# Optimization experiments

Measured on AMD Instinct MI355X. Metric: run time of the kernel, lower is better.

## Reference

```python
import jax, jax.numpy as jnp
import numpy as np


def setup_inputs() -> dict:
    key = jax.random.key(0)
    k1, k2, k3 = jax.random.split(key, 3)
    B, Nin, Din, Nout, Dout = 32, 512, 64, 32, 64
    w_const = float(np.sqrt(Nout / (Din * Nin)))  # weight_init_const from module
    return {
        "input_pose": jax.random.normal(k1, (B, Nin, Din), dtype=jnp.float32),
        "current_act": jax.random.uniform(k2, (B, Nin), dtype=jnp.float32),
        "W": w_const * jax.random.normal(k3, (Nin, Din, Nout, Dout), dtype=jnp.float32),
        "num_iter": 3,
    }


def reference(input_pose, current_act, W, num_iter):
    # input_pose: [B, Nin, Din], current_act: [B, Nin], W: [Nin, Din, Nout, Dout]
    Nin, Din, Nout, Dout = W.shape
    scale = 1.0 / np.sqrt(Dout)

    # Vote projection is iteration-invariant: compute once.  [B, Nin, Nout, Dout]
    votes = jnp.einsum('bna,namd->bnmd', input_pose, W)

    # Initial pass: q0 = softmax(zeros) = uniform 1/Nout over classes.
    # einsum('nm,bna,namd->bmd', q0, pose, W) == votes.sum(n) / Nout
    next_capsule_value = votes.sum(axis=1) / Nout  # [B, Nout, Dout]

    query_key = None
    for _ in range(max(1, num_iter)):
        # 'bna,namd,bmd->bnm' == contraction of cached votes with current class poses
        logits = jnp.einsum('bnmd,bmd->bnm', votes, next_capsule_value) * scale
        query_key = jax.nn.softmax(logits, axis=2)  # [B, Nin, Nout]
        # 'bnm,bna,namd,bn->bmd' == activation-weighted vote aggregation
        next_capsule_value = jnp.einsum('bnm,bnmd,bn->bmd', query_key, votes, current_act)

    # act_type == 'EM' and next_act is None -> pose L2 norm
    next_act = jnp.linalg.norm(next_capsule_value, axis=-1)  # [B, Nout]

    # per-route x per-class interaction embeddings  [B, Nin, Nout, Dout]
    weights = query_key * current_act[..., None]
    route_class_emb = weights[..., None] * votes

    return next_capsule_value, next_act, query_key, route_class_emb
```

## Files before the change

kernel.cpp:

```cpp
#include <hip/hip_runtime.h>

#define B_    32
#define NIN   512
#define DIN   64
#define NOUT  32
#define DOUT  64
#define NUM_ITER 3

__global__ __launch_bounds__(128) void k_votes(const float* __restrict__ pose,
                                               const float* __restrict__ W,
                                               float* __restrict__ votes) {
    const int n = blockIdx.x >> 5;
    const int m = blockIdx.x & 31;
    const int tid = threadIdx.x;
    const int d4 = tid & 15;
    const int bq = tid >> 4;

    __shared__ float poseL[B_ * 68];
#pragma unroll
    for (int k = 0; k < 4; ++k) {
        int j = tid + k * 128;
        int b = j >> 4, a4 = j & 15;
        float4 v = *((const float4*)(pose + (size_t)(b * NIN + n) * DIN) + a4);
        *(float4*)&poseL[b * 68 + a4 * 4] = v;
    }
    __syncthreads();

    const float4* wp = (const float4*)W + (size_t)n * 32768 + m * 16 + d4;
    const float* p0 = &poseL[(bq * 4 + 0) * 68];
    const float* p1 = p0 + 68;
    const float* p2 = p1 + 68;
    const float* p3 = p2 + 68;

    float4 a0 = {0.f,0.f,0.f,0.f}, a1 = {0.f,0.f,0.f,0.f};
    float4 a2 = {0.f,0.f,0.f,0.f}, a3 = {0.f,0.f,0.f,0.f};
#pragma unroll 16
    for (int a = 0; a < 64; ++a) {
        float4 wv = wp[(size_t)a * 512];
        float q0 = p0[a], q1 = p1[a], q2 = p2[a], q3 = p3[a];
        a0.x = fmaf(q0, wv.x, a0.x); a0.y = fmaf(q0, wv.y, a0.y);
        a0.z = fmaf(q0, wv.z, a0.z); a0.w = fmaf(q0, wv.w, a0.w);
        a1.x = fmaf(q1, wv.x, a1.x); a1.y = fmaf(q1, wv.y, a1.y);
        a1.z = fmaf(q1, wv.z, a1.z); a1.w = fmaf(q1, wv.w, a1.w);
        a2.x = fmaf(q2, wv.x, a2.x); a2.y = fmaf(q2, wv.y, a2.y);
        a2.z = fmaf(q2, wv.z, a2.z); a2.w = fmaf(q2, wv.w, a2.w);
        a3.x = fmaf(q3, wv.x, a3.x); a3.y = fmaf(q3, wv.y, a3.y);
        a3.z = fmaf(q3, wv.z, a3.z); a3.w = fmaf(q3, wv.w, a3.w);
    }
    float4* vo = (float4*)votes + ((size_t)(bq * 4) * NIN + n) * 512 + m * 16 + d4;
    const size_t bs = (size_t)NIN * 512;
    vo[0]      = a0;
    vo[bs]     = a1;
    vo[2 * bs] = a2;
    vo[3 * bs] = a3;
}

__global__ __launch_bounds__(256) void k_ncv0(const float* __restrict__ votes,
                                              float* __restrict__ ncv) {
    int gid = blockIdx.x * 256 + threadIdx.x;
    int nc = gid >> 16;
    int e  = gid & 65535;
    int b  = e >> 11;
    int r  = e & 2047;
    const float* vp = votes + (size_t)b * (NIN * 2048) + (size_t)nc * 64 * 2048 + r;
    float s = 0.f;
#pragma unroll 8
    for (int nn = 0; nn < 64; ++nn) s += vp[nn * 2048];
    atomicAdd(&ncv[e], s * (1.0f / NOUT));
}

__global__ __launch_bounds__(256) void k_iter(float* __restrict__ votes,
                                              const float* __restrict__ act,
                                              const float* __restrict__ ncv_in,
                                              float* __restrict__ ncv_out,
                                              float* __restrict__ qk_out,
                                              int last) {
    const int b = blockIdx.x >> 5;
    const int chunk = blockIdx.x & 31;
    const int tid = threadIdx.x;
    const int wave = tid >> 6, lane = tid & 63;
    const int m = lane & 31, half = lane >> 5;
    const int sl = m * 64 + half * 32;

    const float4* np = (const float4*)(ncv_in + (size_t)b * 2048 + sl);
    float4 ncvs[8];
#pragma unroll
    for (int i = 0; i < 8; ++i) ncvs[i] = np[i];

    float4 acc[8];
#pragma unroll
    for (int i = 0; i < 8; ++i) acc[i] = make_float4(0.f, 0.f, 0.f, 0.f);

    const int n0 = chunk * 16 + wave * 4;

    for (int nn = 0; nn < 4; ++nn) {
        const int n = n0 + nn;
        float4* vp = (float4*)(votes + (size_t)(b * NIN + n) * 2048 + sl);
        float4 v[8];
#pragma unroll
        for (int i = 0; i < 8; ++i) v[i] = vp[i];

        float part = 0.f;
#pragma unroll
        for (int i = 0; i < 8; ++i) {
            part = fmaf(v[i].x, ncvs[i].x, part);
            part = fmaf(v[i].y, ncvs[i].y, part);
            part = fmaf(v[i].z, ncvs[i].z, part);
            part = fmaf(v[i].w, ncvs[i].w, part);
        }
        part += __shfl_xor(part, 32);
        float lg = part * 0.125f;

        float mx = lg;
#pragma unroll
        for (int off = 16; off >= 1; off >>= 1) mx = fmaxf(mx, __shfl_xor(mx, off));
        float e = __expf(lg - mx);
        float s = e;
#pragma unroll
        for (int off = 16; off >= 1; off >>= 1) s += __shfl_xor(s, off);
        float qk = e / s;
        if (half == 0) qk_out[(size_t)(b * NIN + n) * NOUT + m] = qk;

        const float qa = qk * act[b * NIN + n];
#pragma unroll
        for (int i = 0; i < 8; ++i) {
            acc[i].x = fmaf(qa, v[i].x, acc[i].x);
            acc[i].y = fmaf(qa, v[i].y, acc[i].y);
            acc[i].z = fmaf(qa, v[i].z, acc[i].z);
            acc[i].w = fmaf(qa, v[i].w, acc[i].w);
        }
        if (last) {
#pragma unroll
            for (int i = 0; i < 8; ++i) {
                float4 ev;
                ev.x = qa * v[i].x; ev.y = qa * v[i].y;
                ev.z = qa * v[i].z; ev.w = qa * v[i].w;
                vp[i] = ev;
            }
        }
    }

    __shared__ float accW[4][64 * 33];
    const int lid = m * 2 + half;
    float* aw = &accW[wave][lid * 33];
#pragma unroll
    for (int i = 0; i < 8; ++i) {
        aw[4 * i + 0] = acc[i].x; aw[4 * i + 1] = acc[i].y;
        aw[4 * i + 2] = acc[i].z; aw[4 * i + 3] = acc[i].w;
    }
    __syncthreads();
    for (int e = tid; e < 2048; e += 256) {
        int mm = e >> 6, dd = e & 63;
        int idx = (mm * 2 + (dd >> 5)) * 33 + (dd & 31);
        float s = accW[0][idx] + accW[1][idx] + accW[2][idx] + accW[3][idx];
        atomicAdd(&ncv_out[(size_t)b * 2048 + e], s);
    }
}

__global__ __launch_bounds__(256) void k_final_ncv(const float* __restrict__ ncv,
                                                   float* __restrict__ ncv_out,
                                                   float* __restrict__ act_out) {
    int gid = blockIdx.x * 256 + threadIdx.x;
    ncv_out[gid] = ncv[gid];
    if (gid < B_ * NOUT) {
        const float* p = ncv + gid * DOUT;
        float s = 0.f;
#pragma unroll 8
        for (int d = 0; d < DOUT; ++d) s = fmaf(p[d], p[d], s);
        act_out[gid] = sqrtf(s);
    }
}

extern "C" void kernel_launch(void* const* d_in, const int* in_sizes, int n_in,
                              void* d_out, int out_size, void* d_ws, size_t ws_size,
                              hipStream_t stream) {
    const float* pose = (const float*)d_in[0];
    const float* act  = (const float*)d_in[1];
    const float* W    = (const float*)d_in[2];

    float* out = (float*)d_out;
    float* ncv_out = out;
    float* act_out = out + 65536;
    float* qk_out  = out + 66560;
    float* emb_out = out + 590848;

    char* ws = (char*)d_ws;
    float* ncvA = (float*)ws;
    float* ncvB = (float*)(ws + 262144);

    float* votes = emb_out;

    k_votes<<<NIN * NOUT, 128, 0, stream>>>(pose, W, votes);

    hipMemsetAsync(ncvA, 0, B_ * NOUT * DOUT * sizeof(float), stream);
    k_ncv0<<<2048, 256, 0, stream>>>(votes, ncvA);

    float* cur = ncvA;
    float* nxt = ncvB;
    for (int it = 0; it < NUM_ITER; ++it) {
        hipMemsetAsync(nxt, 0, B_ * NOUT * DOUT * sizeof(float), stream);
        k_iter<<<B_ * 32, 256, 0, stream>>>(votes, act, cur, nxt, qk_out,
                                            it == NUM_ITER - 1 ? 1 : 0);
        float* t = cur; cur = nxt; nxt = t;
    }

    k_final_ncv<<<256, 256, 0, stream>>>(cur, ncv_out, act_out);
}
```

Before: 617.6 us.

## Retile vote projection kernel by capsule and batch group with larger register tiles

The votes kernel now gives each block one input capsule and a group of 8 batch elements covering all 32 output classes. Each thread computes an 8-batch by 8-dim register tile and loads the pose vector as float4. The block index is permuted so blocks sharing the same n (and thus the same W slice) run on different XCDs or close in time. W is now read four times per capsule instead of once per (n,m) block over all 32 batches, trading W reuse for fewer blocks and larger per-thread tiles, with higher register pressure.

Result: faster. 585.4 us (-5.2%).

```diff
diff --git a/kernel.cpp b/kernel.cpp
--- a/kernel.cpp
+++ b/kernel.cpp
@@ -7,52 +7,71 @@
 #define DOUT  64
 #define NUM_ITER 3
 
-__global__ __launch_bounds__(128) void k_votes(const float* __restrict__ pose,
+__global__ __launch_bounds__(256) void k_votes(const float* __restrict__ pose,
                                                const float* __restrict__ W,
                                                float* __restrict__ votes) {
-    const int n = blockIdx.x >> 5;
-    const int m = blockIdx.x & 31;
+    const int logical = (blockIdx.x & 7) * 256 + (blockIdx.x >> 3);
+    const int n  = logical >> 2;
+    const int b0 = (logical & 3) * 8;
     const int tid = threadIdx.x;
-    const int d4 = tid & 15;
-    const int bq = tid >> 4;
-
-    __shared__ float poseL[B_ * 68];
-#pragma unroll
-    for (int k = 0; k < 4; ++k) {
-        int j = tid + k * 128;
-        int b = j >> 4, a4 = j & 15;
-        float4 v = *((const float4*)(pose + (size_t)(b * NIN + n) * DIN) + a4);
-        *(float4*)&poseL[b * 68 + a4 * 4] = v;
+    const int m  = tid >> 3;
+    const int d8 = tid & 7;
+
+    __shared__ float poseL[8 * 64];
+    if (tid < 128) {
+        int bb = tid >> 4, a4 = tid & 15;
+        float4 v = *((const float4*)(pose + (size_t)((b0 + bb) * NIN + n) * DIN) + a4);
+        *(float4*)&poseL[bb * 64 + a4 * 4] = v;
     }
     __syncthreads();
 
-    const float4* wp = (const float4*)W + (size_t)n * 32768 + m * 16 + d4;
-    const float* p0 = &poseL[(bq * 4 + 0) * 68];
-    const float* p1 = p0 + 68;
-    const float* p2 = p1 + 68;
-    const float* p3 = p2 + 68;
-
-    float4 a0 = {0.f,0.f,0.f,0.f}, a1 = {0.f,0.f,0.f,0.f};
-    float4 a2 = {0.f,0.f,0.f,0.f}, a3 = {0.f,0.f,0.f,0.f};
-#pragma unroll 16
-    for (int a = 0; a < 64; ++a) {
-        float4 wv = wp[(size_t)a * 512];
-        float q0 = p0[a], q1 = p1[a], q2 = p2[a], q3 = p3[a];
-        a0.x = fmaf(q0, wv.x, a0.x); a0.y = fmaf(q0, wv.y, a0.y);
-        a0.z = fmaf(q0, wv.z, a0.z); a0.w = fmaf(q0, wv.w, a0.w);
-        a1.x = fmaf(q1, wv.x, a1.x); a1.y = fmaf(q1, wv.y, a1.y);
-        a1.z = fmaf(q1, wv.z, a1.z); a1.w = fmaf(q1, wv.w, a1.w);
-        a2.x = fmaf(q2, wv.x, a2.x); a2.y = fmaf(q2, wv.y, a2.y);
-        a2.z = fmaf(q2, wv.z, a2.z); a2.w = fmaf(q2, wv.w, a2.w);
-        a3.x = fmaf(q3, wv.x, a3.x); a3.y = fmaf(q3, wv.y, a3.y);
-        a3.z = fmaf(q3, wv.z, a3.z); a3.w = fmaf(q3, wv.w, a3.w);
-    }
-    float4* vo = (float4*)votes + ((size_t)(bq * 4) * NIN + n) * 512 + m * 16 + d4;
-    const size_t bs = (size_t)NIN * 512;
-    vo[0]      = a0;
-    vo[bs]     = a1;
-    vo[2 * bs] = a2;
-    vo[3 * bs] = a3;
+    const float4* wp = (const float4*)W + (size_t)n * 32768 + m * 16 + d8 * 2;
+
+    float4 acc0[8] = {};
+    float4 acc1[8] = {};
+
+#define CAP_STEP(AA, COMP)                                                  \
+    {                                                                       \
+        _Pragma("unroll")                                                   \
+        for (int bb = 0; bb < 8; ++bb) {                                    \
+            float p = pt[bb].COMP;                                          \
+            acc0[bb].x = fmaf(p, wv[AA][0].x, acc0[bb].x);                  \
+            acc0[bb].y = fmaf(p, wv[AA][0].y, acc0[bb].y);                  \
+            acc0[bb].z = fmaf(p, wv[AA][0].z, acc0[bb].z);                  \
+            acc0[bb].w = fmaf(p, wv[AA][0].w, acc0[bb].w);                  \
+            acc1[bb].x = fmaf(p, wv[AA][1].x, acc1[bb].x);                  \
+            acc1[bb].y = fmaf(p, wv[AA][1].y, acc1[bb].y);                  \
+            acc1[bb].z = fmaf(p, wv[AA][1].z, acc1[bb].z);                  \
+            acc1[bb].w = fmaf(p, wv[AA][1].w, acc1[bb].w);                  \
+        }                                                                   \
+    }
+
+    for (int a0 = 0; a0 < 64; a0 += 4) {
+        float4 wv[4][2];
+#pragma unroll
+        for (int aa = 0; aa < 4; ++aa) {
+            wv[aa][0] = wp[(size_t)(a0 + aa) * 512];
+            wv[aa][1] = wp[(size_t)(a0 + aa) * 512 + 1];
+        }
+        float4 pt[8];
+#pragma unroll
+        for (int bb = 0; bb < 8; ++bb)
+            pt[bb] = *(const float4*)&poseL[bb * 64 + a0];
+
+        CAP_STEP(0, x)
+        CAP_STEP(1, y)
+        CAP_STEP(2, z)
+        CAP_STEP(3, w)
+    }
+#undef CAP_STEP
+
+#pragma unroll
+    for (int bb = 0; bb < 8; ++bb) {
+        float4* vo = (float4*)votes +
+                     ((size_t)((b0 + bb) * NIN + n)) * 512 + m * 16 + d8 * 2;
+        vo[0] = acc0[bb];
+        vo[1] = acc1[bb];
+    }
 }
 
 __global__ __launch_bounds__(256) void k_ncv0(const float* __restrict__ votes,
@@ -190,7 +209,7 @@
 
     float* votes = emb_out;
 
-    k_votes<<<NIN * NOUT, 128, 0, stream>>>(pose, W, votes);
+    k_votes<<<NIN * 4, 256, 0, stream>>>(pose, W, votes);
 
     hipMemsetAsync(ncvA, 0, B_ * NOUT * DOUT * sizeof(float), stream);
     k_ncv0<<<2048, 256, 0, stream>>>(votes, ncvA);
```
